# Performance work log

Hardware: AMD Instinct MI355X
Metric: run time of the kernel (lower is better)

## Reference

```python
import jax, jax.numpy as jnp
import numpy as np

LEVEL = 2
IN_CH = 128
OUT_CH = 128
BASE_MODES = (16, 16)


def haar_dwt(x):
    # x: [B, C, H, W] with even H, W. Orthonormal 2D Haar (db1) analysis.
    x00 = x[:, :, 0::2, 0::2]
    x01 = x[:, :, 0::2, 1::2]
    x10 = x[:, :, 1::2, 0::2]
    x11 = x[:, :, 1::2, 1::2]
    ll = (x00 + x01 + x10 + x11) * 0.5
    lh = (x00 - x01 + x10 - x11) * 0.5  # high-freq along width
    hl = (x00 + x01 - x10 - x11) * 0.5  # high-freq along height
    hh = (x00 - x01 - x10 + x11) * 0.5
    return ll, lh, hl, hh


def haar_idwt(ll, lh, hl, hh):
    # Orthonormal 2D Haar synthesis (exact inverse of haar_dwt).
    x00 = (ll + lh + hl + hh) * 0.5
    x01 = (ll - lh + hl - hh) * 0.5
    x10 = (ll + lh - hl - hh) * 0.5
    x11 = (ll - lh - hl + hh) * 0.5
    b, c, h2, w2 = ll.shape
    row0 = jnp.stack([x00, x01], axis=-1).reshape(b, c, h2, 2 * w2)
    row1 = jnp.stack([x10, x11], axis=-1).reshape(b, c, h2, 2 * w2)
    return jnp.stack([row0, row1], axis=-2).reshape(b, c, 2 * h2, 2 * w2)


def setup_inputs() -> dict:
    key = jax.random.key(0)
    kx, k1, k2, k3, k4 = jax.random.split(key, 5)
    scale = 1.0 / (IN_CH * OUT_CH)
    wshape = (IN_CH, OUT_CH) + BASE_MODES
    x = jax.random.normal(kx, (32, IN_CH, 128, 128), dtype=jnp.float32)
    w1 = scale * jax.random.uniform(k1, wshape, dtype=jnp.float32)
    w2 = scale * jax.random.uniform(k2, wshape, dtype=jnp.float32)
    w3 = scale * jax.random.uniform(k3, wshape, dtype=jnp.float32)
    w4 = scale * jax.random.uniform(k4, wshape, dtype=jnp.float32)
    return {"x": x, "w1": w1, "w2": w2, "w3": w3, "w4": w4}


def reference(x, w1, w2, w3, w4):
    # Multi-level Haar DWT
    ll = x
    coeffs = []  # finest -> coarsest, matching pytorch_wavelets yh ordering
    for _ in range(LEVEL):
        ll, lh, hl, hh = haar_dwt(ll)
        coeffs.append((lh, hl, hh))

    th, tw = ll.shape[-2], ll.shape[-1]

    def interp(w):
        # bilinear, half-pixel centers == torch align_corners=False (upsampling)
        return jax.image.resize(w, w.shape[:2] + (th, tw), method="bilinear")

    def mul2d(a, w):
        return jnp.einsum("bixy,ioxy->boxy", a, interp(w))

    out_ll = mul2d(ll, w1)
    lh, hl, hh = coeffs[-1]  # only coarsest level is mixed; finer levels zeroed
    out = haar_idwt(out_ll, mul2d(lh, w2), mul2d(hl, w3), mul2d(hh, w4))
    for _ in range(LEVEL - 1):
        z = jnp.zeros_like(out)
        out = haar_idwt(out, z, z, z)
    return out
```

## Files before the change

kernel.cpp:

```cpp
#include <hip/hip_runtime.h>
#include <stdint.h>

__device__ __forceinline__ float bf2f(uint32_t v) { return __uint_as_float(v << 16); }
__device__ __forceinline__ uint32_t f2bf(float f) {
  uint32_t u = __float_as_uint(f);
  return (u + 0x7fffu + ((u >> 16) & 1u)) >> 16;
}

__device__ __forceinline__ void interp_coord(int p, int& i0, int& i1, float& f) {
  if (p == 0)       { i0 = 0;  i1 = 0;  f = 0.f; }
  else if (p == 31) { i0 = 15; i1 = 15; f = 0.f; }
  else if (p & 1)   { i0 = (p - 1) >> 1; i1 = i0 + 1; f = 0.25f; }
  else              { i0 = (p >> 1) - 1; i1 = i0 + 1; f = 0.75f; }
}

__global__ __launch_bounds__(256) void dwt_kernel(const float* __restrict__ x,
                                                  uint16_t* __restrict__ bands) {
  __shared__ uint16_t tile[4 * 32 * 34];
  const int bid = blockIdx.x;
  const int cg4 = bid & 3;
  const int h   = (bid >> 2) & 31;
  const int b   = bid >> 7;
  const int t   = threadIdx.x;
  const int w   = t & 31;
  const int cl  = t >> 5;
#pragma unroll
  for (int cc = 0; cc < 4; ++cc) {
    const int c = cl + (cc << 3);
    const float* xc = x + (((size_t)(b << 7) + (cg4 << 5) + c) << 14) + (h << 9) + (w << 2);
    float4 r0 = *(const float4*)(xc);
    float4 r1 = *(const float4*)(xc + 128);
    float4 r2 = *(const float4*)(xc + 256);
    float4 r3 = *(const float4*)(xc + 384);
    float S00 = r0.x + r0.y + r1.x + r1.y;
    float S01 = r0.z + r0.w + r1.z + r1.w;
    float S10 = r2.x + r2.y + r3.x + r3.y;
    float S11 = r2.z + r2.w + r3.z + r3.w;
    tile[(0 * 32 + w) * 34 + c] = (uint16_t)f2bf(0.25f * (S00 + S01 + S10 + S11));
    tile[(1 * 32 + w) * 34 + c] = (uint16_t)f2bf(0.25f * (S00 - S01 + S10 - S11));
    tile[(2 * 32 + w) * 34 + c] = (uint16_t)f2bf(0.25f * (S00 + S01 - S10 - S11));
    tile[(3 * 32 + w) * 34 + c] = (uint16_t)f2bf(0.25f * (S00 - S01 - S10 + S11));
  }
  __syncthreads();
  const uint32_t* tl = (const uint32_t*)tile;
  uint32_t* bo = (uint32_t*)bands;
#pragma unroll
  for (int j = 0; j < 8; ++j) {
    const int idx = t + (j << 8);
    const int k   = idx >> 9;
    const int rem = idx & 511;
    const int w2  = rem >> 4;
    const int qq  = rem & 15;
    const uint32_t v = tl[(k * 32 + w2) * 17 + qq];
    bo[(((size_t)(k << 10) + (h << 5) + w2) << 11) + (b << 6) + (cg4 << 4) + qq] = v;
  }
}

__global__ __launch_bounds__(256) void winterp_kernel(const float* __restrict__ w1,
                                                      const float* __restrict__ w2,
                                                      const float* __restrict__ w3,
                                                      const float* __restrict__ w4,
                                                      uint16_t* __restrict__ W32) {
  __shared__ uint16_t Lw[64 * 258];
  const int bid = blockIdx.x;
  const int k   = bid >> 8;
  const int io0 = (bid & 255) << 6;
  const float* src = (k == 0) ? w1 : (k == 1) ? w2 : (k == 2) ? w3 : w4;
  const int t = threadIdx.x;
  uint32_t* Lwu = (uint32_t*)Lw;
#pragma unroll
  for (int j = 0; j < 16; ++j) {
    const int idx4 = t + (j << 8);
    const int row  = idx4 >> 6;
    const int c4   = idx4 & 63;
    float4 v = *(const float4*)(src + (((size_t)(io0 + row)) << 8) + (c4 << 2));
    Lwu[row * 129 + (c4 << 1)]     = f2bf(v.x) | (f2bf(v.y) << 16);
    Lwu[row * 129 + (c4 << 1) + 1] = f2bf(v.z) | (f2bf(v.w) << 16);
  }
  __syncthreads();
  const int io_l = t & 63;
  const int pg   = t >> 6;
  uint16_t* dst = W32 + ((size_t)k << 24) + io0 + io_l;
  for (int lp = 0; lp < 256; ++lp) {
    const int p = (lp << 2) + pg;
    const int py = p >> 5, px = p & 31;
    int y0, y1, x0, x1; float fy, fx;
    interp_coord(py, y0, y1, fy);
    interp_coord(px, x0, x1, fx);
    const float c00 = (1.f - fy) * (1.f - fx), c01 = (1.f - fy) * fx;
    const float c10 = fy * (1.f - fx),         c11 = fy * fx;
    const float vA = bf2f(Lw[io_l * 258 + (y0 << 4) + x0]);
    const float vB = bf2f(Lw[io_l * 258 + (y0 << 4) + x1]);
    const float vC = bf2f(Lw[io_l * 258 + (y1 << 4) + x0]);
    const float vD = bf2f(Lw[io_l * 258 + (y1 << 4) + x1]);
    dst[(size_t)p << 14] = (uint16_t)f2bf(c00 * vA + c01 * vB + c10 * vC + c11 * vD);
  }
}

__global__ __launch_bounds__(256) void gemm_kernel(const uint16_t* __restrict__ bands,
                                                   const uint16_t* __restrict__ W32,
                                                   uint16_t* __restrict__ ws2) {
  __shared__ uint16_t Ws[16384];
  __shared__ float At[128 * 36];
  const int bid = blockIdx.x;
  const int k = bid & 3;
  const int p = bid >> 2;
  const int t = threadIdx.x;
  const uint4* wsrc = (const uint4*)(W32 + (((size_t)(k << 10) + p) << 14));
  uint4* wdst = (uint4*)Ws;
#pragma unroll
  for (int j = 0; j < 8; ++j) wdst[t + (j << 8)] = wsrc[t + (j << 8)];
  const uint32_t* ab = (const uint32_t*)(bands + (((size_t)(k << 10) + p) << 12));
#pragma unroll
  for (int j = 0; j < 8; ++j) {
    const int idx = t + (j << 8);
    const uint32_t u = ab[idx];
    const int bb = idx >> 6;
    const int i0 = (idx & 63) << 1;
    At[i0 * 36 + bb]       = bf2f(u & 0xffffu);
    At[(i0 + 1) * 36 + bb] = bf2f(u >> 16);
  }
  __syncthreads();
  const int q = t & 31;
  const int g = t >> 5;
  float acc[16];
#pragma unroll
  for (int j = 0; j < 16; ++j) acc[j] = 0.f;
  const uint32_t* WsuC = (const uint32_t*)Ws;
#pragma unroll 8
  for (int i = 0; i < 128; ++i) {
    float4 av = *(const float4*)&At[i * 36 + (g << 2)];
    uint2 wu  = *(const uint2*)&WsuC[(i << 6) + (q << 1)];
    float w0_ = __uint_as_float(wu.x << 16);
    float w1_ = __uint_as_float(wu.x & 0xffff0000u);
    float w2_ = __uint_as_float(wu.y << 16);
    float w3_ = __uint_as_float(wu.y & 0xffff0000u);
    acc[0]  += av.x * w0_; acc[1]  += av.x * w1_; acc[2]  += av.x * w2_; acc[3]  += av.x * w3_;
    acc[4]  += av.y * w0_; acc[5]  += av.y * w1_; acc[6]  += av.y * w2_; acc[7]  += av.y * w3_;
    acc[8]  += av.z * w0_; acc[9]  += av.z * w1_; acc[10] += av.z * w2_; acc[11] += av.z * w3_;
    acc[12] += av.w * w0_; acc[13] += av.w * w1_; acc[14] += av.w * w2_; acc[15] += av.w * w3_;
  }
  uint32_t* wout = (uint32_t*)(ws2 + (((size_t)(k << 10) + p) << 12));
#pragma unroll
  for (int db = 0; db < 4; ++db) {
    const int b = (g << 2) + db;
    uint32_t u01 = f2bf(acc[db * 4 + 0]) | (f2bf(acc[db * 4 + 1]) << 16);
    uint32_t u23 = f2bf(acc[db * 4 + 2]) | (f2bf(acc[db * 4 + 3]) << 16);
    *(uint2*)&wout[b * 64 + (q << 1)] = make_uint2(u01, u23);
  }
}

__global__ __launch_bounds__(256) void idwt_kernel(const uint16_t* __restrict__ ws2,
                                                   float* __restrict__ out) {
  __shared__ uint16_t Ls[4 * 32 * 130];
  const int bid = blockIdx.x;
  const int b = bid >> 5;
  const int h = bid & 31;
  const int t = threadIdx.x;
  const uint32_t* su = (const uint32_t*)ws2;
  uint32_t* Lu = (uint32_t*)Ls;
#pragma unroll 4
  for (int j = 0; j < 32; ++j) {
    const int idx = t + (j << 8);
    const int kw = idx >> 6;
    const int uo = idx & 63;
    const int k = kw >> 5, w = kw & 31;
    const uint32_t v = su[(((size_t)(k << 10) + (h << 5) + w) << 11) + (b << 6) + uo];
    Lu[kw * 65 + uo] = v;
  }
  __syncthreads();
  const int x4 = t & 31;
  const int og = t >> 5;
  for (int pp = 0; pp < 16; ++pp) {
    const int o = (pp << 3) + og;
    const float A = bf2f(Ls[(0 * 32 + x4) * 130 + o]);
    const float B = bf2f(Ls[(1 * 32 + x4) * 130 + o]);
    const float C = bf2f(Ls[(2 * 32 + x4) * 130 + o]);
    const float D = bf2f(Ls[(3 * 32 + x4) * 130 + o]);
    const float E = A + B, F = A - B, G = C + D, Hh = C - D;
    const float vL0 = 0.25f * (E + G),  vR0 = 0.25f * (F + Hh);
    const float vL1 = 0.25f * (E - G),  vR1 = 0.25f * (F - Hh);
    float* ob = out + (((size_t)(b << 7) + o) << 14) + (h << 9) + (x4 << 2);
    float4 top = make_float4(vL0, vL0, vR0, vR0);
    float4 bot = make_float4(vL1, vL1, vR1, vR1);
    *(float4*)(ob)       = top;
    *(float4*)(ob + 128) = top;
    *(float4*)(ob + 256) = bot;
    *(float4*)(ob + 384) = bot;
  }
}

extern "C" void kernel_launch(void* const* d_in, const int* in_sizes, int n_in,
                              void* d_out, int out_size, void* d_ws, size_t ws_size,
                              hipStream_t stream) {
  const float* x  = (const float*)d_in[0];
  const float* w1 = (const float*)d_in[1];
  const float* w2 = (const float*)d_in[2];
  const float* w3 = (const float*)d_in[3];
  const float* w4 = (const float*)d_in[4];

  uint16_t* bands = (uint16_t*)d_ws;
  uint16_t* ws2   = bands + (size_t)16777216;
  uint16_t* W32 = (uint16_t*)d_out;

  dwt_kernel<<<4096, 256, 0, stream>>>(x, bands);
  winterp_kernel<<<1024, 256, 0, stream>>>(w1, w2, w3, w4, W32);
  gemm_kernel<<<4096, 256, 0, stream>>>(bands, W32, ws2);
  idwt_kernel<<<1024, 256, 0, stream>>>(ws2, (float*)d_out);
}
```

Measured before the change: 655.6 us.

## Fuse weight interpolation into MFMA GEMM and repack weights to bf16 compact layout

Replaces the full 32x32 interpolated weight materialization with a compact bf16 repack of the 16x16 base weights laid out [k][yx][o][i]. The GEMM kernel now performs the bilinear interpolation on the fly from four neighbouring base-weight slices while staging into LDS, then computes the per-mode 32x128x128 product with bf16 MFMA 16x16x32 instructions instead of scalar FP32 FMAs. This removes the large interpolated-weight write and read and moves the contraction onto matrix cores. The cost is four gathered weight reads per block and an LDS round trip to transpose the output.

```diff
diff --git a/kernel.cpp b/kernel.cpp
--- a/kernel.cpp
+++ b/kernel.cpp
@@ -13,6 +13,9 @@
   else if (p & 1)   { i0 = (p - 1) >> 1; i1 = i0 + 1; f = 0.25f; }
   else              { i0 = (p >> 1) - 1; i1 = i0 + 1; f = 0.75f; }
 }
+
+typedef short bf16x8 __attribute__((ext_vector_type(8)));
+typedef float f32x4 __attribute__((ext_vector_type(4)));
 
 __global__ __launch_bounds__(256) void dwt_kernel(const float* __restrict__ x,
                                                   uint16_t* __restrict__ bands) {
@@ -56,97 +59,125 @@
   }
 }
 
-__global__ __launch_bounds__(256) void winterp_kernel(const float* __restrict__ w1,
+__global__ __launch_bounds__(256) void wrepack_kernel(const float* __restrict__ w1,
                                                       const float* __restrict__ w2,
                                                       const float* __restrict__ w3,
                                                       const float* __restrict__ w4,
-                                                      uint16_t* __restrict__ W32) {
-  __shared__ uint16_t Lw[64 * 258];
-  const int bid = blockIdx.x;
-  const int k   = bid >> 8;
-  const int io0 = (bid & 255) << 6;
+                                                      uint16_t* __restrict__ wr) {
+  __shared__ uint16_t L[64 * 262];
+  const int bid = blockIdx.x;
+  const int k = bid >> 7;
+  const int o = bid & 127;
   const float* src = (k == 0) ? w1 : (k == 1) ? w2 : (k == 2) ? w3 : w4;
   const int t = threadIdx.x;
-  uint32_t* Lwu = (uint32_t*)Lw;
-#pragma unroll
-  for (int j = 0; j < 16; ++j) {
-    const int idx4 = t + (j << 8);
-    const int row  = idx4 >> 6;
-    const int c4   = idx4 & 63;
-    float4 v = *(const float4*)(src + (((size_t)(io0 + row)) << 8) + (c4 << 2));
-    Lwu[row * 129 + (c4 << 1)]     = f2bf(v.x) | (f2bf(v.y) << 16);
-    Lwu[row * 129 + (c4 << 1) + 1] = f2bf(v.z) | (f2bf(v.w) << 16);
-  }
-  __syncthreads();
-  const int io_l = t & 63;
-  const int pg   = t >> 6;
-  uint16_t* dst = W32 + ((size_t)k << 24) + io0 + io_l;
-  for (int lp = 0; lp < 256; ++lp) {
-    const int p = (lp << 2) + pg;
-    const int py = p >> 5, px = p & 31;
-    int y0, y1, x0, x1; float fy, fx;
-    interp_coord(py, y0, y1, fy);
-    interp_coord(px, x0, x1, fx);
-    const float c00 = (1.f - fy) * (1.f - fx), c01 = (1.f - fy) * fx;
-    const float c10 = fy * (1.f - fx),         c11 = fy * fx;
-    const float vA = bf2f(Lw[io_l * 258 + (y0 << 4) + x0]);
-    const float vB = bf2f(Lw[io_l * 258 + (y0 << 4) + x1]);
-    const float vC = bf2f(Lw[io_l * 258 + (y1 << 4) + x0]);
-    const float vD = bf2f(Lw[io_l * 258 + (y1 << 4) + x1]);
-    dst[(size_t)p << 14] = (uint16_t)f2bf(c00 * vA + c01 * vB + c10 * vC + c11 * vD);
+  uint32_t* Lu = (uint32_t*)L;
+  for (int ih = 0; ih < 2; ++ih) {
+    if (ih) __syncthreads();
+#pragma unroll
+    for (int j = 0; j < 16; ++j) {
+      const int ridx = t + (j << 8);
+      const int il = ridx >> 6;
+      const int x4 = ridx & 63;
+      float4 v = *(const float4*)(src + (((size_t)((ih * 64 + il) * 128 + o)) << 8) + (x4 << 2));
+      Lu[il * 131 + (x4 << 1)]     = f2bf(v.x) | (f2bf(v.y) << 16);
+      Lu[il * 131 + (x4 << 1) + 1] = f2bf(v.z) | (f2bf(v.w) << 16);
+    }
+    __syncthreads();
+#pragma unroll
+    for (int j = 0; j < 32; ++j) {
+      const int oidx = t + (j << 8);
+      const int yx = oidx >> 5;
+      const int q  = oidx & 31;
+      const uint32_t lo = L[(q << 1) * 262 + yx];
+      const uint32_t hi = L[((q << 1) + 1) * 262 + yx];
+      uint32_t* dst = (uint32_t*)wr + (((size_t)(k << 8) + yx) << 13) + (o << 6) + (ih << 5) + q;
+      *dst = lo | (hi << 16);
+    }
   }
 }
 
 __global__ __launch_bounds__(256) void gemm_kernel(const uint16_t* __restrict__ bands,
-                                                   const uint16_t* __restrict__ W32,
+                                                   const uint16_t* __restrict__ wr,
                                                    uint16_t* __restrict__ ws2) {
-  __shared__ uint16_t Ws[16384];
-  __shared__ float At[128 * 36];
+  __shared__ uint16_t Wt[128 * 136];
   const int bid = blockIdx.x;
   const int k = bid & 3;
   const int p = bid >> 2;
   const int t = threadIdx.x;
-  const uint4* wsrc = (const uint4*)(W32 + (((size_t)(k << 10) + p) << 14));
-  uint4* wdst = (uint4*)Ws;
-#pragma unroll
-  for (int j = 0; j < 8; ++j) wdst[t + (j << 8)] = wsrc[t + (j << 8)];
-  const uint32_t* ab = (const uint32_t*)(bands + (((size_t)(k << 10) + p) << 12));
+  const int py = p >> 5, px = p & 31;
+  int y0, y1, x0, x1; float fy, fx;
+  interp_coord(py, y0, y1, fy);
+  interp_coord(px, x0, x1, fx);
+  const float c00 = (1.f - fy) * (1.f - fx), c01 = (1.f - fy) * fx;
+  const float c10 = fy * (1.f - fx),         c11 = fy * fx;
+  const uint16_t* wk = wr + ((size_t)k << 22);
+  const uint4* rA = (const uint4*)(wk + (((size_t)(y0 << 4) + x0) << 14));
+  const uint4* rB = (const uint4*)(wk + (((size_t)(y0 << 4) + x1) << 14));
+  const uint4* rC = (const uint4*)(wk + (((size_t)(y1 << 4) + x0) << 14));
+  const uint4* rD = (const uint4*)(wk + (((size_t)(y1 << 4) + x1) << 14));
+  uint32_t* Wtu = (uint32_t*)Wt;
+#pragma unroll
+  for (int j = 0; j < 8; ++j) {
+    const int fi = t + (j << 8);
+    const int o  = fi >> 4;
+    const int i8 = fi & 15;
+    const uint4 a = rA[fi], b = rB[fi], c = rC[fi], d = rD[fi];
+    uint32_t ou[4];
+#pragma unroll
+    for (int cc = 0; cc < 4; ++cc) {
+      const uint32_t ua = (&a.x)[cc], ub = (&b.x)[cc], uc = (&c.x)[cc], ud = (&d.x)[cc];
+      float lo = c00 * __uint_as_float(ua << 16) + c01 * __uint_as_float(ub << 16)
+               + c10 * __uint_as_float(uc << 16) + c11 * __uint_as_float(ud << 16);
+      float hi = c00 * __uint_as_float(ua & 0xffff0000u) + c01 * __uint_as_float(ub & 0xffff0000u)
+               + c10 * __uint_as_float(uc & 0xffff0000u) + c11 * __uint_as_float(ud & 0xffff0000u);
+      ou[cc] = f2bf(lo) | (f2bf(hi) << 16);
+    }
+    *(uint4*)(Wtu + o * 68 + (i8 << 2)) = make_uint4(ou[0], ou[1], ou[2], ou[3]);
+  }
+  __syncthreads();
+  const int wv = t >> 6;
+  const int l  = t & 63;
+  const int lr = l & 15;
+  const int lk = (l >> 4) << 3;
+  const uint16_t* gA = bands + (((size_t)(k << 10) + p) << 12);
+  bf16x8 af[2][4], bg[2][4];
+#pragma unroll
+  for (int s = 0; s < 4; ++s) {
+#pragma unroll
+    for (int m = 0; m < 2; ++m)
+      af[m][s] = *(const bf16x8*)(gA + (((m << 4) + lr) << 7) + (s << 5) + lk);
+#pragma unroll
+    for (int n = 0; n < 2; ++n)
+      bg[n][s] = *(const bf16x8*)(&Wt[((wv << 5) + (n << 4) + lr) * 136 + (s << 5) + lk]);
+  }
+  f32x4 acc[2][2] = {};
+#pragma unroll
+  for (int s = 0; s < 4; ++s)
+#pragma unroll
+    for (int m = 0; m < 2; ++m)
+#pragma unroll
+      for (int n = 0; n < 2; ++n)
+        acc[m][n] = __builtin_amdgcn_mfma_f32_16x16x32_bf16(af[m][s], bg[n][s], acc[m][n], 0, 0, 0);
+  __syncthreads();
+  uint16_t* Ds = Wt;
+#pragma unroll
+  for (int m = 0; m < 2; ++m)
+#pragma unroll
+    for (int n = 0; n < 2; ++n)
+#pragma unroll
+      for (int r = 0; r < 4; ++r) {
+        const int b_ = (m << 4) + ((l >> 4) << 2) + r;
+        const int o_ = (wv << 5) + (n << 4) + lr;
+        Ds[b_ * 136 + o_] = (uint16_t)f2bf(acc[m][n][r]);
+      }
+  __syncthreads();
+  uint32_t* outp = (uint32_t*)(ws2 + (((size_t)(k << 10) + p) << 12));
+  const uint32_t* Dsu = (const uint32_t*)Ds;
 #pragma unroll
   for (int j = 0; j < 8; ++j) {
     const int idx = t + (j << 8);
-    const uint32_t u = ab[idx];
-    const int bb = idx >> 6;
-    const int i0 = (idx & 63) << 1;
-    At[i0 * 36 + bb]       = bf2f(u & 0xffffu);
-    At[(i0 + 1) * 36 + bb] = bf2f(u >> 16);
-  }
-  __syncthreads();
-  const int q = t & 31;
-  const int g = t >> 5;
-  float acc[16];
-#pragma unroll
-  for (int j = 0; j < 16; ++j) acc[j] = 0.f;
-  const uint32_t* WsuC = (const uint32_t*)Ws;
-#pragma unroll 8
-  for (int i = 0; i < 128; ++i) {
-    float4 av = *(const float4*)&At[i * 36 + (g << 2)];
-    uint2 wu  = *(const uint2*)&WsuC[(i << 6) + (q << 1)];
-    float w0_ = __uint_as_float(wu.x << 16);
-    float w1_ = __uint_as_float(wu.x & 0xffff0000u);
-    float w2_ = __uint_as_float(wu.y << 16);
-    float w3_ = __uint_as_float(wu.y & 0xffff0000u);
-    acc[0]  += av.x * w0_; acc[1]  += av.x * w1_; acc[2]  += av.x * w2_; acc[3]  += av.x * w3_;
-    acc[4]  += av.y * w0_; acc[5]  += av.y * w1_; acc[6]  += av.y * w2_; acc[7]  += av.y * w3_;
-    acc[8]  += av.z * w0_; acc[9]  += av.z * w1_; acc[10] += av.z * w2_; acc[11] += av.z * w3_;
-    acc[12] += av.w * w0_; acc[13] += av.w * w1_; acc[14] += av.w * w2_; acc[15] += av.w * w3_;
-  }
-  uint32_t* wout = (uint32_t*)(ws2 + (((size_t)(k << 10) + p) << 12));
-#pragma unroll
-  for (int db = 0; db < 4; ++db) {
-    const int b = (g << 2) + db;
-    uint32_t u01 = f2bf(acc[db * 4 + 0]) | (f2bf(acc[db * 4 + 1]) << 16);
-    uint32_t u23 = f2bf(acc[db * 4 + 2]) | (f2bf(acc[db * 4 + 3]) << 16);
-    *(uint2*)&wout[b * 64 + (q << 1)] = make_uint2(u01, u23);
+    const int b_ = idx >> 6, c_ = idx & 63;
+    outp[idx] = Dsu[b_ * 68 + c_];
   }
 }
 
@@ -201,10 +232,10 @@
 
   uint16_t* bands = (uint16_t*)d_ws;
   uint16_t* ws2   = bands + (size_t)16777216;
-  uint16_t* W32 = (uint16_t*)d_out;
-
+  uint16_t* wr = (uint16_t*)d_out;
+
+  wrepack_kernel<<<512, 256, 0, stream>>>(w1, w2, w3, w4, wr);
   dwt_kernel<<<4096, 256, 0, stream>>>(x, bands);
-  winterp_kernel<<<1024, 256, 0, stream>>>(w1, w2, w3, w4, W32);
-  gemm_kernel<<<4096, 256, 0, stream>>>(bands, W32, ws2);
+  gemm_kernel<<<4096, 256, 0, stream>>>(bands, wr, ws2);
   idwt_kernel<<<1024, 256, 0, stream>>>(ws2, (float*)d_out);
 }
```

Result: faster. 557.5 us (-15.0%).
